# Performance work log

Measured on AMD Instinct MI355X. Metric: run time of the kernel, lower is better.

The kernel has to match this reference:

```python
import jax, jax.numpy as jnp
import numpy as np
from jax import lax

R = 2  # upscale factor


def setup_inputs() -> dict:
    key = jax.random.key(0)
    k1, k2, k3 = jax.random.split(key, 3)
    x = jax.random.normal(k1, (16, 192, 192, 64), dtype=jnp.float32)
    # Conv2D kernel: HWIO, filters = r*r*64 = 256
    W = jax.random.normal(k2, (3, 3, 64, 256), dtype=jnp.float32) * 0.05
    b = jax.random.normal(k3, (256,), dtype=jnp.float32) * 0.05
    return {"x": x, "W": W, "b": b}


def reference(x, W, b):
    # Conv2D, stride 1, 'same' padding, NHWC/HWIO
    y = lax.conv_general_dilated(
        x, W, window_strides=(1, 1), padding="SAME",
        dimension_numbers=("NHWC", "HWIO", "NHWC")) + b
    # phase_shift: O[B, i*r+q, j*r+p, k] = y[B, i, j, k*r*r + p*r + q]
    B, a, bdim, c = y.shape
    cp = c // (R * R)
    y = y.reshape(B, a, bdim, cp, R, R)          # [B,a,b,k,p,q]
    y = jnp.transpose(y, (0, 1, 5, 2, 4, 3))     # [B,a,q,b,p,k]
    return y.reshape(B, a * R, bdim * R, cp)
```

## Files before the change

kernel.cpp:

```cpp
#include <hip/hip_runtime.h>
#include <stdint.h>

typedef short bf16x8 __attribute__((ext_vector_type(8)));
typedef float f32x4  __attribute__((ext_vector_type(4)));

#define GLOAD_LDS16(gp, lp) \
    __builtin_amdgcn_global_load_lds((const __attribute__((address_space(1))) void*)(gp), \
                                     (__attribute__((address_space(3))) void*)(lp), 16, 0, 0)

__device__ __forceinline__ uint32_t bfbits(float f) {
    uint32_t u = __builtin_bit_cast(uint32_t, f);
    u += 0x7FFFu + ((u >> 16) & 1u);
    return u >> 16;
}
__device__ __forceinline__ uint32_t pk2(float a, float b) {
    return bfbits(a) | (bfbits(b) << 16);
}

__global__ void prep_kernel(const float* __restrict__ x, short* __restrict__ xb,
                            const float* __restrict__ W, short* __restrict__ Wt) {
    const int b = blockIdx.x;
    if (b < 2048) {
        const int total = 16 * 194 * 194 * 8;
        for (int i = b * 256 + threadIdx.x; i < total; i += 2048 * 256) {
            int g  = i & 7;
            int t  = i >> 3;
            int wp = t % 194; t /= 194;
            int hp = t % 194;
            int nn = t / 194;
            uint4 r = {0u, 0u, 0u, 0u};
            if (hp >= 1 && hp <= 192 && wp >= 1 && wp <= 192) {
                const float* s = x + (((size_t)nn * 192 + (hp - 1)) * 192 + (wp - 1)) * 64 + g * 8;
                f32x4 a = __builtin_nontemporal_load((const f32x4*)s);
                f32x4 bb = __builtin_nontemporal_load((const f32x4*)(s + 4));
                r.x = pk2(a[0], a[1]); r.y = pk2(a[2], a[3]);
                r.z = pk2(bb[0], bb[1]); r.w = pk2(bb[2], bb[3]);
            }
            *(uint4*)(xb + (size_t)i * 8) = r;
        }
    } else {
        int idx = (b - 2048) * 256 + threadIdx.x;
        if (idx < 147456) {
            int t  = idx >> 14;
            int r  = idx & 16383;
            int c  = r >> 12;
            int j  = (r >> 6) & 63;
            int ic = r & 63;
            Wt[idx] = (short)bfbits(W[(t * 64 + ic) * 256 + j * 4 + c]);
        }
    }
}

#define NRING 7
#define ASLOT_B 8448
#define B_OFF   (NRING * ASLOT_B)
#define SMEM_SHORTS ((B_OFF + 2 * 8192) / 2)

__global__ __launch_bounds__(256, 2) void conv_ps_kernel(
    const short* __restrict__ xb, const short* __restrict__ Wt,
    const float* __restrict__ bias, float* __restrict__ out)
{
    __shared__ short smem[SMEM_SHORTS];

    const int tid   = threadIdx.x;
    const int lane  = tid & 63;
    const int wv    = tid >> 6;
    const int row_l = lane & 15;
    const int grp   = lane >> 4;
    const int b7    = row_l & 7;

    const int raw = blockIdx.x;
    const int lb  = (raw & 7) * 192 + (raw >> 3);
    const int c    = lb & 3;
    const int wt   = (lb >> 2) % 3;
    const int hseg = (lb / 12) % 8;
    const int n    = lb / 96;
    const int w0   = wt * 64;
    const int hbase = hseg * 24;
    const int q = c & 1, p = (c >> 1) & 1;

    const short* wsrc = Wt + c * 4096;

    auto issueB = [&](int tap, int buf) {
        #pragma unroll
        for (int r = 0; r < 2; ++r) {
            int cch = tid + r * 256;
            int j = cch >> 3, s = cch & 7, ss = s ^ (j & 7);
            GLOAD_LDS16(wsrc + tap * 16384 + j * 64 + ss * 8,
                        (char*)smem + B_OFF + buf * 8192 + (wv * 64 + r * 256) * 16);
        }
    };
    auto issueA = [&](int row) {
        int rowc = row > 192 ? 192 : row;
        int slot = (row + 1) % NRING;
        size_t rbase = ((size_t)n * 194 + (rowc + 1)) * 194;
        #pragma unroll
        for (int r = 0; r < 2; ++r) {
            int cch = wv * 132 + r * 64 + lane;
            int wpos = cch >> 3, g = cch & 7, gs = g ^ (wpos & 7);
            GLOAD_LDS16(xb + (rbase + (w0 + wpos)) * 64 + gs * 8,
                        (char*)smem + slot * ASLOT_B + (wv * 132 + r * 64) * 16);
        }
        if (lane < 4) {
            int cch = wv * 132 + 128 + lane;
            int wpos = cch >> 3, g = cch & 7, gs = g ^ (wpos & 7);
            GLOAD_LDS16(xb + (rbase + (w0 + wpos)) * 64 + gs * 8,
                        (char*)smem + slot * ASLOT_B + (wv * 132 + 128) * 16);
        }
    };

    issueB(0, 0);
    #pragma unroll
    for (int r = 0; r < 5; ++r) issueA(hbase - 1 + r);
    asm volatile("s_waitcnt vmcnt(0)" ::: "memory");
    __builtin_amdgcn_sched_barrier(0);
    __syncthreads();

    f32x4 bv4[4];
    #pragma unroll
    for (int nt = 0; nt < 4; ++nt) {
        const int j0 = nt * 16 + grp * 4;
        #pragma unroll
        for (int jv = 0; jv < 4; ++jv)
            bv4[nt][jv] = bias[(j0 + jv) * 4 + c];
    }

    f32x4 accA[4][4], accB[4][4];
    bf16x8 af0[2][4], af1[2][4];

#define SCHB __builtin_amdgcn_sched_barrier(0)

#define READ_AF(DST, SLOT, DX) { \
    const int rd_ = row_l + (DX); \
    const int a7_ = rd_ & 7; \
    const int aB_ = (SLOT) * 4224 + rd_ * 64; \
    _Pragma("unroll") for (int ks = 0; ks < 2; ++ks) { \
        const short* ap_ = &smem[aB_ + (((ks * 4 + grp) ^ a7_) << 3)]; \
        _Pragma("unroll") for (int mt_ = 0; mt_ < 4; ++mt_) \
            DST[ks][mt_] = *(const bf16x8*)(ap_ + mt_ * 1024); \
    } }

#define ST2(ACCO, S) { \
    const int mt_ = (S) >> 1, n0_ = ((S) & 1) * 2; \
    float* po_ = out + ((rowb_o + 2 * (w0 + mt_ * 16 + row_l) + p) * 64 + grp * 4); \
    __builtin_nontemporal_store(ACCO[mt_][n0_],     (f32x4*)(po_ + n0_ * 16)); \
    __builtin_nontemporal_store(ACCO[mt_][n0_ + 1], (f32x4*)(po_ + (n0_ + 1) * 16)); }

#define TAPX(ACC, K, PAR, VM, EXTRA, STS, AFC, AFN, NSLOT, NDX) \
    __builtin_amdgcn_s_barrier(); SCHB; \
    issueB(((K) + 1) % 9, ((PAR) + (K) + 1) & 1); \
    EXTRA; SCHB; \
    STS; SCHB; \
    asm volatile("s_waitcnt vmcnt(" #VM ")" ::: "memory"); SCHB; \
    __builtin_amdgcn_s_barrier(); SCHB; \
    { \
        bf16x8 bfr[2][4]; \
        const short* bbase_ = smem + B_OFF / 2 + ((((PAR) + (K)) & 1)) * 4096 + row_l * 64; \
        _Pragma("unroll") for (int ks = 0; ks < 2; ++ks) { \
            const short* bp_ = bbase_ + (((ks * 4 + grp) ^ b7) << 3); \
            _Pragma("unroll") for (int nt_ = 0; nt_ < 4; ++nt_) \
                bfr[ks][nt_] = *(const bf16x8*)(bp_ + nt_ * 1024); \
        } \
        READ_AF(AFN, NSLOT, NDX); \
        _Pragma("unroll") for (int ks = 0; ks < 2; ++ks) \
            _Pragma("unroll") for (int mt_ = 0; mt_ < 4; ++mt_) \
                _Pragma("unroll") for (int nt_ = 0; nt_ < 4; ++nt_) \
                    ACC[mt_][nt_] = __builtin_amdgcn_mfma_f32_16x16x32_bf16( \
                        bfr[ks][nt_], AFC[ks][mt_], ACC[mt_][nt_], 0, 0, 0); \
    }

#define TILE_HEAD(ACC, ITV) \
    const int h0 = hbase + (ITV) * 4; \
    int sl[3]; \
    _Pragma("unroll") for (int dy = 0; dy < 3; ++dy) sl[dy] = (h0 + wv + dy) % NRING; \
    const int nsl0 = (h0 + 4 + wv) % NRING; \
    (void)nsl0; \
    _Pragma("unroll") for (int i = 0; i < 4; ++i) \
        _Pragma("unroll") for (int j = 0; j < 4; ++j) ACC[i][j] = bv4[j];

#define STEADY_TILE(ACC, ACCO, ITV, PAR, AFE, AFO) { \
    TILE_HEAD(ACC, ITV); \
    const long rowb_o = ((long)(n * 384 + 2 * (h0 - 4 + wv) + q)) * 384; \
    TAPX(ACC, 0, PAR, 10, { issueA(h0 + 4); issueA(h0 + 5); }, ST2(ACCO, 0), AFE, AFO, sl[0], 1); \
    TAPX(ACC, 1, PAR, 12, {}, ST2(ACCO, 1), AFO, AFE, sl[0], 2); \
    TAPX(ACC, 2, PAR,  6, {}, ST2(ACCO, 2), AFE, AFO, sl[1], 0); \
    TAPX(ACC, 3, PAR,  9, { issueA(h0 + 6); }, ST2(ACCO, 3), AFO, AFE, sl[1], 1); \
    TAPX(ACC, 4, PAR,  9, {}, ST2(ACCO, 4), AFE, AFO, sl[1], 2); \
    TAPX(ACC, 5, PAR,  6, {}, ST2(ACCO, 5), AFO, AFE, sl[2], 0); \
    TAPX(ACC, 6, PAR,  9, { issueA(h0 + 7); }, ST2(ACCO, 6), AFE, AFO, sl[2], 1); \
    TAPX(ACC, 7, PAR,  9, {}, ST2(ACCO, 7), AFO, AFE, sl[2], 2); \
    TAPX(ACC, 8, PAR,  4, {}, {}, AFE, AFO, nsl0, 0); }

    {
        const int psl = (hbase + wv) % NRING;
        READ_AF(af0, psl, 0);
    }

    {
        TILE_HEAD(accA, 0);
        TAPX(accA, 0, 0, 8, { issueA(h0 + 4); issueA(h0 + 5); }, {}, af0, af1, sl[0], 1);
        TAPX(accA, 1, 0, 8, {}, {}, af1, af0, sl[0], 2);
        TAPX(accA, 2, 0, 2, {}, {}, af0, af1, sl[1], 0);
        TAPX(accA, 3, 0, 5, { issueA(h0 + 6); }, {}, af1, af0, sl[1], 1);
        TAPX(accA, 4, 0, 5, {}, {}, af0, af1, sl[1], 2);
        TAPX(accA, 5, 0, 2, {}, {}, af1, af0, sl[2], 0);
        TAPX(accA, 6, 0, 5, { issueA(h0 + 7); }, {}, af0, af1, sl[2], 1);
        TAPX(accA, 7, 0, 5, {}, {}, af1, af0, sl[2], 2);
        TAPX(accA, 8, 0, 2, {}, {}, af0, af1, nsl0, 0);
    }
    #pragma unroll 1
    for (int it2 = 1; it2 < 5; it2 += 2) {
        STEADY_TILE(accB, accA, it2, 1, af1, af0);
        STEADY_TILE(accA, accB, it2 + 1, 0, af0, af1);
    }
    STEADY_TILE(accB, accA, 5, 1, af1, af0);
    {
        const int h = hbase + 20 + wv;
        const long rowb = ((long)(n * 384 + 2 * h + q)) * 384;
        #pragma unroll
        for (int mt = 0; mt < 4; ++mt) {
            float* po = out + ((rowb + 2 * (w0 + mt * 16 + row_l) + p) * 64 + grp * 4);
            #pragma unroll
            for (int nt = 0; nt < 4; ++nt)
                __builtin_nontemporal_store(accB[mt][nt], (f32x4*)(po + nt * 16));
        }
    }
#undef STEADY_TILE
#undef TILE_HEAD
#undef TAPX
#undef ST2
#undef READ_AF
#undef SCHB
}

extern "C" void kernel_launch(void* const* d_in, const int* in_sizes, int n_in,
                              void* d_out, int out_size, void* d_ws, size_t ws_size,
                              hipStream_t stream) {
    const float* x = (const float*)d_in[0];
    const float* W = (const float*)d_in[1];
    const float* b = (const float*)d_in[2];
    float* out = (float*)d_out;

    const size_t xb_bytes = (size_t)16 * 194 * 194 * 64 * 2;
    short* xbuf = (short*)d_ws;
    short* Wt   = (short*)((char*)d_ws + xb_bytes);

    hipLaunchKernelGGL(prep_kernel, dim3(2624), dim3(256), 0, stream, x, xbuf, W, Wt);
    hipLaunchKernelGGL(conv_ps_kernel, dim3(1536), dim3(256), 0, stream, xbuf, Wt, b, out);
}
```

Before: 234.1 us.

## Load conv weights directly into registers and cut per-tap LDS barriers

Weight fragments are now read straight from global memory into registers, double-buffered per K-half, instead of being staged through LDS with async loads. The activation ring grows from 7 to 9 row slots so more rows are prefetched ahead, which lets each tile use one mid-tile barrier and one boundary barrier instead of two barriers per tap. The goal is to remove LDS traffic and synchronisation stalls in the MFMA loop. In exchange each wave issues its own redundant global loads of the weights (served by cache), and register pressure rises.

After: 372.1 us. 1.59x slower.

```diff
diff --git a/kernel.cpp b/kernel.cpp
--- a/kernel.cpp
+++ b/kernel.cpp
@@ -51,10 +51,9 @@
     }
 }
 
-#define NRING 7
+#define NRING 9
 #define ASLOT_B 8448
-#define B_OFF   (NRING * ASLOT_B)
-#define SMEM_SHORTS ((B_OFF + 2 * 8192) / 2)
+#define SMEM_SHORTS (NRING * ASLOT_B / 2)
 
 __global__ __launch_bounds__(256, 2) void conv_ps_kernel(
     const short* __restrict__ xb, const short* __restrict__ Wt,
@@ -67,7 +66,6 @@
     const int wv    = tid >> 6;
     const int row_l = lane & 15;
     const int grp   = lane >> 4;
-    const int b7    = row_l & 7;
 
     const int raw = blockIdx.x;
     const int lb  = (raw & 7) * 192 + (raw >> 3);
@@ -81,15 +79,6 @@
 
     const short* wsrc = Wt + c * 4096;
 
-    auto issueB = [&](int tap, int buf) {
-        #pragma unroll
-        for (int r = 0; r < 2; ++r) {
-            int cch = tid + r * 256;
-            int j = cch >> 3, s = cch & 7, ss = s ^ (j & 7);
-            GLOAD_LDS16(wsrc + tap * 16384 + j * 64 + ss * 8,
-                        (char*)smem + B_OFF + buf * 8192 + (wv * 64 + r * 256) * 16);
-        }
-    };
     auto issueA = [&](int row) {
         int rowc = row > 192 ? 192 : row;
         int slot = (row + 1) % NRING;
@@ -109,9 +98,19 @@
         }
     };
 
-    issueB(0, 0);
-    #pragma unroll
-    for (int r = 0; r < 5; ++r) issueA(hbase - 1 + r);
+    bf16x8 bb0[4], bb1[4];
+
+#define LOADB(DST, T, KS) { \
+    const short* bp_ = wsrcv + (T) * 16384 + row_l * 64 + ((KS) * 4 + grp) * 8; \
+    _Pragma("unroll") for (int nt_ = 0; nt_ < 4; ++nt_) \
+        DST[nt_] = *(const bf16x8*)(bp_ + nt_ * 1024); }
+
+    {
+        const short* wsrcv = wsrc;
+        #pragma unroll
+        for (int r = 0; r < 6; ++r) issueA(hbase - 1 + r);
+        LOADB(bb0, 0, 0);
+    }
     asm volatile("s_waitcnt vmcnt(0)" ::: "memory");
     __builtin_amdgcn_sched_barrier(0);
     __syncthreads();
@@ -126,19 +125,26 @@
     }
 
     f32x4 accA[4][4], accB[4][4];
-    bf16x8 af0[2][4], af1[2][4];
 
 #define SCHB __builtin_amdgcn_sched_barrier(0)
-
-#define READ_AF(DST, SLOT, DX) { \
+#define MIDBAR  SCHB; __builtin_amdgcn_s_barrier(); SCHB;
+#define BOUND   SCHB; asm volatile("s_waitcnt vmcnt(16)" ::: "memory"); SCHB; \
+                __builtin_amdgcn_s_barrier(); SCHB;
+
+#define PHX(ACC, DY, DX, KS, BCUR, DOLD, BNXT, NT_, NK_, EXTRA, STS) { \
+    EXTRA; \
+    STS; \
+    if (DOLD) LOADB(BNXT, NT_, NK_); \
     const int rd_ = row_l + (DX); \
     const int a7_ = rd_ & 7; \
-    const int aB_ = (SLOT) * 4224 + rd_ * 64; \
-    _Pragma("unroll") for (int ks = 0; ks < 2; ++ks) { \
-        const short* ap_ = &smem[aB_ + (((ks * 4 + grp) ^ a7_) << 3)]; \
-        _Pragma("unroll") for (int mt_ = 0; mt_ < 4; ++mt_) \
-            DST[ks][mt_] = *(const bf16x8*)(ap_ + mt_ * 1024); \
-    } }
+    const short* ap_ = &smem[sl[DY] * 4224 + rd_ * 64 + ((((KS) * 4 + grp) ^ a7_) << 3)]; \
+    bf16x8 af_[4]; \
+    _Pragma("unroll") for (int mt_ = 0; mt_ < 4; ++mt_) \
+        af_[mt_] = *(const bf16x8*)(ap_ + mt_ * 1024); \
+    _Pragma("unroll") for (int mt_ = 0; mt_ < 4; ++mt_) \
+        _Pragma("unroll") for (int nt_ = 0; nt_ < 4; ++nt_) \
+            ACC[mt_][nt_] = __builtin_amdgcn_mfma_f32_16x16x32_bf16( \
+                BCUR[nt_], af_[mt_], ACC[mt_][nt_], 0, 0, 0); }
 
 #define ST2(ACCO, S) { \
     const int mt_ = (S) >> 1, n0_ = ((S) & 1) * 2; \
@@ -146,74 +152,48 @@
     __builtin_nontemporal_store(ACCO[mt_][n0_],     (f32x4*)(po_ + n0_ * 16)); \
     __builtin_nontemporal_store(ACCO[mt_][n0_ + 1], (f32x4*)(po_ + (n0_ + 1) * 16)); }
 
-#define TAPX(ACC, K, PAR, VM, EXTRA, STS, AFC, AFN, NSLOT, NDX) \
-    __builtin_amdgcn_s_barrier(); SCHB; \
-    issueB(((K) + 1) % 9, ((PAR) + (K) + 1) & 1); \
-    EXTRA; SCHB; \
-    STS; SCHB; \
-    asm volatile("s_waitcnt vmcnt(" #VM ")" ::: "memory"); SCHB; \
-    __builtin_amdgcn_s_barrier(); SCHB; \
-    { \
-        bf16x8 bfr[2][4]; \
-        const short* bbase_ = smem + B_OFF / 2 + ((((PAR) + (K)) & 1)) * 4096 + row_l * 64; \
-        _Pragma("unroll") for (int ks = 0; ks < 2; ++ks) { \
-            const short* bp_ = bbase_ + (((ks * 4 + grp) ^ b7) << 3); \
-            _Pragma("unroll") for (int nt_ = 0; nt_ < 4; ++nt_) \
-                bfr[ks][nt_] = *(const bf16x8*)(bp_ + nt_ * 1024); \
-        } \
-        READ_AF(AFN, NSLOT, NDX); \
-        _Pragma("unroll") for (int ks = 0; ks < 2; ++ks) \
-            _Pragma("unroll") for (int mt_ = 0; mt_ < 4; ++mt_) \
-                _Pragma("unroll") for (int nt_ = 0; nt_ < 4; ++nt_) \
-                    ACC[mt_][nt_] = __builtin_amdgcn_mfma_f32_16x16x32_bf16( \
-                        bfr[ks][nt_], AFC[ks][mt_], ACC[mt_][nt_], 0, 0, 0); \
-    }
-
 #define TILE_HEAD(ACC, ITV) \
     const int h0 = hbase + (ITV) * 4; \
+    uint64_t wadr_ = (uint64_t)wsrc; \
+    asm volatile("" : "+s"(wadr_)); \
+    const short* wsrcv = (const short*)wadr_;    \
     int sl[3]; \
     _Pragma("unroll") for (int dy = 0; dy < 3; ++dy) sl[dy] = (h0 + wv + dy) % NRING; \
-    const int nsl0 = (h0 + 4 + wv) % NRING; \
-    (void)nsl0; \
     _Pragma("unroll") for (int i = 0; i < 4; ++i) \
         _Pragma("unroll") for (int j = 0; j < 4; ++j) ACC[i][j] = bv4[j];
 
-#define STEADY_TILE(ACC, ACCO, ITV, PAR, AFE, AFO) { \
+#define GTILE(ACC, ACCO, ITV, DOST, DORF, DOBD) { \
     TILE_HEAD(ACC, ITV); \
     const long rowb_o = ((long)(n * 384 + 2 * (h0 - 4 + wv) + q)) * 384; \
-    TAPX(ACC, 0, PAR, 10, { issueA(h0 + 4); issueA(h0 + 5); }, ST2(ACCO, 0), AFE, AFO, sl[0], 1); \
-    TAPX(ACC, 1, PAR, 12, {}, ST2(ACCO, 1), AFO, AFE, sl[0], 2); \
-    TAPX(ACC, 2, PAR,  6, {}, ST2(ACCO, 2), AFE, AFO, sl[1], 0); \
-    TAPX(ACC, 3, PAR,  9, { issueA(h0 + 6); }, ST2(ACCO, 3), AFO, AFE, sl[1], 1); \
-    TAPX(ACC, 4, PAR,  9, {}, ST2(ACCO, 4), AFE, AFO, sl[1], 2); \
-    TAPX(ACC, 5, PAR,  6, {}, ST2(ACCO, 5), AFO, AFE, sl[2], 0); \
-    TAPX(ACC, 6, PAR,  9, { issueA(h0 + 7); }, ST2(ACCO, 6), AFE, AFO, sl[2], 1); \
-    TAPX(ACC, 7, PAR,  9, {}, ST2(ACCO, 7), AFO, AFE, sl[2], 2); \
-    TAPX(ACC, 8, PAR,  4, {}, {}, AFE, AFO, nsl0, 0); }
-
-    {
-        const int psl = (hbase + wv) % NRING;
-        READ_AF(af0, psl, 0);
-    }
-
-    {
-        TILE_HEAD(accA, 0);
-        TAPX(accA, 0, 0, 8, { issueA(h0 + 4); issueA(h0 + 5); }, {}, af0, af1, sl[0], 1);
-        TAPX(accA, 1, 0, 8, {}, {}, af1, af0, sl[0], 2);
-        TAPX(accA, 2, 0, 2, {}, {}, af0, af1, sl[1], 0);
-        TAPX(accA, 3, 0, 5, { issueA(h0 + 6); }, {}, af1, af0, sl[1], 1);
-        TAPX(accA, 4, 0, 5, {}, {}, af0, af1, sl[1], 2);
-        TAPX(accA, 5, 0, 2, {}, {}, af1, af0, sl[2], 0);
-        TAPX(accA, 6, 0, 5, { issueA(h0 + 7); }, {}, af0, af1, sl[2], 1);
-        TAPX(accA, 7, 0, 5, {}, {}, af1, af0, sl[2], 2);
-        TAPX(accA, 8, 0, 2, {}, {}, af0, af1, nsl0, 0);
-    }
+    PHX(ACC,0,0,0, bb0,1,bb1,0,1, if (DORF) issueA(h0 + 5), {}); \
+    PHX(ACC,0,0,1, bb1,1,bb0,1,0, if (DORF) issueA(h0 + 6), if (DOST) ST2(ACCO,0)); \
+    PHX(ACC,0,1,0, bb0,1,bb1,1,1, if (DORF) issueA(h0 + 7), {}); \
+    PHX(ACC,0,1,1, bb1,1,bb0,2,0, {}, if (DOST) ST2(ACCO,1)); \
+    PHX(ACC,0,2,0, bb0,1,bb1,2,1, {}, {}); \
+    PHX(ACC,0,2,1, bb1,1,bb0,3,0, {}, if (DOST) ST2(ACCO,2)); \
+    MIDBAR;    \
+    PHX(ACC,1,0,0, bb0,1,bb1,3,1, if (DORF) issueA(h0 + 8), {}); \
+    PHX(ACC,1,0,1, bb1,1,bb0,4,0, {}, if (DOST) ST2(ACCO,3)); \
+    PHX(ACC,1,1,0, bb0,1,bb1,4,1, {}, {}); \
+    PHX(ACC,1,1,1, bb1,1,bb0,5,0, {}, if (DOST) ST2(ACCO,4)); \
+    PHX(ACC,1,2,0, bb0,1,bb1,5,1, {}, {}); \
+    PHX(ACC,1,2,1, bb1,1,bb0,6,0, {}, if (DOST) ST2(ACCO,5)); \
+    PHX(ACC,2,0,0, bb0,1,bb1,6,1, {}, {}); \
+    PHX(ACC,2,0,1, bb1,1,bb0,7,0, {}, if (DOST) ST2(ACCO,6)); \
+    PHX(ACC,2,1,0, bb0,1,bb1,7,1, {}, {}); \
+    PHX(ACC,2,1,1, bb1,1,bb0,8,0, {}, if (DOST) ST2(ACCO,7)); \
+    PHX(ACC,2,2,0, bb0,1,bb1,8,1, {}, {}); \
+    PHX(ACC,2,2,1, bb1,DOBD,bb0,0,0, {}, {}); \
+    if (DOBD) { BOUND; } }
+
+    GTILE(accA, accB, 0, 0, 1, 1);
     #pragma unroll 1
     for (int it2 = 1; it2 < 5; it2 += 2) {
-        STEADY_TILE(accB, accA, it2, 1, af1, af0);
-        STEADY_TILE(accA, accB, it2 + 1, 0, af0, af1);
-    }
-    STEADY_TILE(accB, accA, 5, 1, af1, af0);
+        GTILE(accB, accA, it2,     1, 1, 1);
+        GTILE(accA, accB, it2 + 1, 1, 1, 1);
+    }
+    GTILE(accB, accA, 5, 1, 0, 0);
+
     {
         const int h = hbase + 20 + wv;
         const long rowb = ((long)(n * 384 + 2 * h + q)) * 384;
@@ -225,12 +205,14 @@
                 __builtin_nontemporal_store(accB[mt][nt], (f32x4*)(po + nt * 16));
         }
     }
-#undef STEADY_TILE
+#undef GTILE
 #undef TILE_HEAD
-#undef TAPX
 #undef ST2
-#undef READ_AF
+#undef PHX
+#undef BOUND
+#undef MIDBAR
 #undef SCHB
+#undef LOADB
 }
 
 extern "C" void kernel_launch(void* const* d_in, const int* in_sizes, int n_in,
```
